# Optimization experiments

Measured on AMD Instinct MI355X. Metric: run time of the kernel, lower is better.

Reference implementation:

```python
import jax, jax.numpy as jnp
import numpy as np

N = 8192
D_IN = 512
D_OUT = 64
ALPHA = 0.2  # LeakyReLU negative slope
MASK_VAL = -9e15


def setup_inputs() -> dict:
    key = jax.random.key(0)
    k1, k2, k3, k4 = jax.random.split(key, 4)
    inp = jax.random.normal(k1, (N, D_IN), dtype=jnp.float32)
    adj = (jax.random.uniform(k2, (N, N)) < 0.05).astype(jnp.float32)
    adj = adj.at[jnp.arange(N), jnp.arange(N)].set(1.0)
    W = jax.random.normal(k3, (D_IN, D_OUT), dtype=jnp.float32) * 0.05
    a = jax.random.normal(k4, (2 * D_OUT, 1), dtype=jnp.float32) * 0.05
    return {"input": inp, "adj": adj, "W": W, "a": a}


def reference(input, adj, W, a):
    # h = input @ W : [n, out]
    h = input @ W
    # Algebraic equivalent of the dense pairwise concat:
    # e_ij = leakyrelu([h_i || h_j] . a) = leakyrelu(h_i.a1 + h_j.a2)
    a1, a2 = a[:D_OUT, 0], a[D_OUT:, 0]          # [out], [out]
    e = jax.nn.leaky_relu(
        (h @ a1)[:, None] + (h @ a2)[None, :],    # [n, n]
        negative_slope=ALPHA,
    )
    attention = jnp.where(adj > 0, e, MASK_VAL)
    attention = jax.nn.softmax(attention, axis=1)
    out = attention @ h                            # [n, out]
    return jax.nn.elu(out)                         # end=False branch
```

## Files before the change

kernel.cpp:

```cpp
#include <hip/hip_runtime.h>
#include <hip/hip_bf16.h>

#define N 8192
#define D_IN 512
#define D_OUT 64
#define ALPHA 0.2f
#define CAP 640
#define RPW 8

__global__ __launch_bounds__(256) void gat_h_kernel(
    const float* __restrict__ input, const float* __restrict__ W,
    const float* __restrict__ a, float* __restrict__ h,
    float* __restrict__ s1, float* __restrict__ s2)
{
    int wave = (blockIdx.x * 256 + threadIdx.x) >> 6;
    int lane = threadIdx.x & 63;
    int row0 = wave * RPW;
    const float* in0 = input + (size_t)row0 * D_IN;
    float a1 = a[lane], a2 = a[D_OUT + lane];
    float acc[RPW];
#pragma unroll
    for (int r = 0; r < RPW; ++r) acc[r] = 0.f;
#pragma unroll 4
    for (int k = 0; k < D_IN; ++k) {
        float wk = W[k * D_OUT + lane];
#pragma unroll
        for (int r = 0; r < RPW; ++r)
            acc[r] = fmaf(in0[(size_t)r * D_IN + k], wk, acc[r]);
    }
#pragma unroll
    for (int r = 0; r < RPW; ++r) {
        h[((size_t)(row0 + r) << 6) + lane] = acc[r];
        float p1 = acc[r] * a1;
        float p2 = acc[r] * a2;
#pragma unroll
        for (int off = 32; off; off >>= 1) {
            p1 += __shfl_xor(p1, off, 64);
            p2 += __shfl_xor(p2, off, 64);
        }
        if (lane == 0) { s1[row0 + r] = p1; s2[row0 + r] = p2; }
    }
}

__global__ __launch_bounds__(256) void gat_attn_kernel(
    const float* __restrict__ adj, const float* __restrict__ h,
    const float* __restrict__ s1, const float* __restrict__ s2,
    float* __restrict__ out)
{
    __shared__ uint2 nbr[4][CAP];
    int wid  = (blockIdx.x * 256 + threadIdx.x) >> 6;
    int lane = threadIdx.x & 63;
    int ws   = threadIdx.x >> 6;
    const float4* adj_row = (const float4*)(adj + (size_t)wid * N);
    const float4* s2v     = (const float4*)s2;
    float s1i  = s1[wid];
    float eref = s1i + s2[wid];
    eref = eref > 0.f ? eref : ALPHA * eref;
    float lsum = 0.f;
    int base = 0;

    float4 av = adj_row[lane];
    float4 sv = s2v[lane];
    for (int j0 = 0; j0 < N; j0 += 256) {
        float4 avn, svn;
        bool more = (j0 + 256) < N;
        if (more) {
            int o = ((j0 + 256) >> 2) + lane;
            avn = adj_row[o];
            svn = s2v[o];
        }
#pragma unroll
        for (int z = 0; z < 4; ++z) {
            bool nb = (&av.x)[z] > 0.f;
            float e = s1i + (&sv.x)[z];
            e = e > 0.f ? e : ALPHA * e;
            float w = nb ? __expf(e - eref) : 0.f;
            lsum += w;
            unsigned long long m = __ballot(nb);
            if (nb) {
                int prefix = __builtin_amdgcn_mbcnt_hi(
                    (unsigned)(m >> 32),
                    __builtin_amdgcn_mbcnt_lo((unsigned)m, 0u));
                nbr[ws][base + prefix] =
                    make_uint2((unsigned)(j0 + (lane << 2) + z), __float_as_uint(w));
            }
            base += __popcll(m);
        }
        if (more) { av = avn; sv = svn; }
    }
#pragma unroll
    for (int off = 32; off; off >>= 1) lsum += __shfl_xor(lsum, off, 64);

    int cnt = base;
    float acc0 = 0.f, acc1 = 0.f, acc2 = 0.f, acc3 = 0.f;
    int nb8 = cnt & ~7;
    uint2 cur[8];
    if (nb8) {
#pragma unroll
        for (int t = 0; t < 8; ++t) cur[t] = nbr[ws][t];
    }
    for (int k = 0; k < nb8; k += 8) {
        float wv[8], hv[8];
#pragma unroll
        for (int t = 0; t < 8; ++t) {
            int j = __builtin_amdgcn_readfirstlane((int)cur[t].x);
            wv[t] = __uint_as_float(cur[t].y);
            hv[t] = h[((size_t)j << 6) + lane];
        }
        if (k + 8 < nb8) {
#pragma unroll
            for (int t = 0; t < 8; ++t) cur[t] = nbr[ws][k + 8 + t];
        }
#pragma unroll
        for (int t = 0; t < 8; ++t) {
            float v = fmaf(wv[t], hv[t], (t & 3) == 0 ? acc0 : (t & 3) == 1 ? acc1
                                        : (t & 3) == 2 ? acc2 : acc3);
            if ((t & 3) == 0) acc0 = v; else if ((t & 3) == 1) acc1 = v;
            else if ((t & 3) == 2) acc2 = v; else acc3 = v;
        }
    }
    for (int k = nb8; k < cnt; ++k) {
        uint2 e = nbr[ws][k];
        int j = __builtin_amdgcn_readfirstlane((int)e.x);
        acc0 = fmaf(__uint_as_float(e.y), h[((size_t)j << 6) + lane], acc0);
    }
    float o = ((acc0 + acc1) + (acc2 + acc3)) / lsum;
    out[((size_t)wid << 6) + lane] = o > 0.f ? o : expm1f(o);
}

extern "C" void kernel_launch(void* const* d_in, const int* in_sizes, int n_in,
                              void* d_out, int out_size, void* d_ws, size_t ws_size,
                              hipStream_t stream) {
    const float* input = (const float*)d_in[0];
    const float* adj   = (const float*)d_in[1];
    const float* W     = (const float*)d_in[2];
    const float* a     = (const float*)d_in[3];
    float* out = (float*)d_out;

    float* h  = (float*)d_ws;
    float* s1 = h + (size_t)N * D_OUT;
    float* s2 = s1 + N;

    gat_h_kernel<<<N / (RPW * 4), 256, 0, stream>>>(input, W, a, h, s1, s2);
    gat_attn_kernel<<<N / 4, 256, 0, stream>>>(adj, h, s1, s2, out);
}
```

Before: 133.3 us.

## Split each attention row across four waves with shared-memory reduction

The attention kernel now assigns one block per row, and each of its four waves scans a 2048-column segment of the adjacency row. Each wave gathers its own compacted neighbor list, and partial accumulators and softmax sums are combined through shared memory after a barrier. The goal is more parallelism and shorter per-wave serial gathers. The h kernel also processes fewer rows per wave. Per-segment neighbor storage is capped at 176 entries, and anything beyond that is silently dropped from the numerator but not from lsum. That is a correctness risk if a segment is denser than expected.

```diff
diff --git a/kernel.cpp b/kernel.cpp
--- a/kernel.cpp
+++ b/kernel.cpp
@@ -5,8 +5,8 @@
 #define D_IN 512
 #define D_OUT 64
 #define ALPHA 0.2f
-#define CAP 640
-#define RPW 8
+#define SEG 176
+#define RPW 4
 
 __global__ __launch_bounds__(256) void gat_h_kernel(
     const float* __restrict__ input, const float* __restrict__ W,
@@ -47,24 +47,29 @@
     const float* __restrict__ s1, const float* __restrict__ s2,
     float* __restrict__ out)
 {
-    __shared__ uint2 nbr[4][CAP];
-    int wid  = (blockIdx.x * 256 + threadIdx.x) >> 6;
+    __shared__ uint2 seg[4][SEG];
+    __shared__ float racc[4][64];
+    __shared__ float rls[4];
+
+    int row  = blockIdx.x;
     int lane = threadIdx.x & 63;
     int ws   = threadIdx.x >> 6;
-    const float4* adj_row = (const float4*)(adj + (size_t)wid * N);
+
+    const float4* adj_row = (const float4*)(adj + (size_t)row * N);
     const float4* s2v     = (const float4*)s2;
-    float s1i  = s1[wid];
-    float eref = s1i + s2[wid];
+    float s1i  = s1[row];
+    float eref = s1i + s2[row];
     eref = eref > 0.f ? eref : ALPHA * eref;
+
     float lsum = 0.f;
-    int base = 0;
-
-    float4 av = adj_row[lane];
-    float4 sv = s2v[lane];
-    for (int j0 = 0; j0 < N; j0 += 256) {
+    int cnt = 0;
+    int cbase = ws << 11;
+    float4 av = adj_row[(cbase >> 2) + lane];
+    float4 sv = s2v[(cbase >> 2) + lane];
+    for (int t = 0; t < 8; ++t) {
+        int j0 = cbase + (t << 8);
         float4 avn, svn;
-        bool more = (j0 + 256) < N;
-        if (more) {
+        if (t < 7) {
             int o = ((j0 + 256) >> 2) + lane;
             avn = adj_row[o];
             svn = s2v[o];
@@ -81,23 +86,25 @@
                 int prefix = __builtin_amdgcn_mbcnt_hi(
                     (unsigned)(m >> 32),
                     __builtin_amdgcn_mbcnt_lo((unsigned)m, 0u));
-                nbr[ws][base + prefix] =
-                    make_uint2((unsigned)(j0 + (lane << 2) + z), __float_as_uint(w));
+                int idx = cnt + prefix;
+                if (idx < SEG)
+                    seg[ws][idx] =
+                        make_uint2((unsigned)(j0 + (lane << 2) + z), __float_as_uint(w));
             }
-            base += __popcll(m);
+            cnt += __popcll(m);
         }
-        if (more) { av = avn; sv = svn; }
+        if (t < 7) { av = avn; sv = svn; }
     }
+    if (cnt > SEG) cnt = SEG;
 #pragma unroll
     for (int off = 32; off; off >>= 1) lsum += __shfl_xor(lsum, off, 64);
 
-    int cnt = base;
     float acc0 = 0.f, acc1 = 0.f, acc2 = 0.f, acc3 = 0.f;
     int nb8 = cnt & ~7;
     uint2 cur[8];
     if (nb8) {
 #pragma unroll
-        for (int t = 0; t < 8; ++t) cur[t] = nbr[ws][t];
+        for (int t = 0; t < 8; ++t) cur[t] = seg[ws][t];
     }
     for (int k = 0; k < nb8; k += 8) {
         float wv[8], hv[8];
@@ -109,7 +116,7 @@
         }
         if (k + 8 < nb8) {
 #pragma unroll
-            for (int t = 0; t < 8; ++t) cur[t] = nbr[ws][k + 8 + t];
+            for (int t = 0; t < 8; ++t) cur[t] = seg[ws][k + 8 + t];
         }
 #pragma unroll
         for (int t = 0; t < 8; ++t) {
@@ -120,12 +127,20 @@
         }
     }
     for (int k = nb8; k < cnt; ++k) {
-        uint2 e = nbr[ws][k];
+        uint2 e = seg[ws][k];
         int j = __builtin_amdgcn_readfirstlane((int)e.x);
         acc0 = fmaf(__uint_as_float(e.y), h[((size_t)j << 6) + lane], acc0);
     }
-    float o = ((acc0 + acc1) + (acc2 + acc3)) / lsum;
-    out[((size_t)wid << 6) + lane] = o > 0.f ? o : expm1f(o);
+
+    racc[ws][lane] = (acc0 + acc1) + (acc2 + acc3);
+    if (lane == 0) rls[ws] = lsum;
+    __syncthreads();
+    if (ws == 0) {
+        float acc = (racc[0][lane] + racc[1][lane]) + (racc[2][lane] + racc[3][lane]);
+        float l = (rls[0] + rls[1]) + (rls[2] + rls[3]);
+        float o = acc / l;
+        out[((size_t)row << 6) + lane] = o > 0.f ? o : expm1f(o);
+    }
 }
 
 extern "C" void kernel_launch(void* const* d_in, const int* in_sizes, int n_in,
@@ -142,5 +157,5 @@
     float* s2 = s1 + N;
 
     gat_h_kernel<<<N / (RPW * 4), 256, 0, stream>>>(input, W, a, h, s1, s2);
-    gat_attn_kernel<<<N / 4, 256, 0, stream>>>(adj, h, s1, s2, out);
+    gat_attn_kernel<<<N, 256, 0, stream>>>(adj, h, s1, s2, out);
 }
```

After: 143.3 us. 7.5% more time.
